# Kernel optimization log

Hardware: AMD Instinct MI355X
Metric: run time of the kernel (lower is better)

The kernel has to match this reference:

```python
import jax, jax.numpy as jnp
import numpy as np

B, V, E, L = 1024, 50000, 256, 17  # batch, nodeNum(vocab), embeddingSize, Huffman path length


def setup_inputs() -> dict:
    key = jax.random.key(0)
    k1, k2, k3, k4, k5 = jax.random.split(key, 5)
    x = jax.random.normal(k1, (B, V), dtype=jnp.float32)
    W = jax.random.normal(k2, (E, V), dtype=jnp.float32) * 0.02  # nn.Linear(nodeNum, embeddingSize).weight
    b = jax.random.normal(k3, (E,), dtype=jnp.float32) * 0.02    # nn.Linear bias
    path_vectors = jax.random.normal(k4, (B, L, E), dtype=jnp.float32)  # gathered treeNode.vector along each target's path
    path_signs = jax.random.randint(k5, (B, L), 0, 2, dtype=jnp.int32)  # 1 == 'left' (+v), 0 == 'right' (-v)
    return {"x": x, "W": W, "b": b, "path_vectors": path_vectors, "path_signs": path_signs}


def reference(x, W, b, path_vectors, path_signs):
    # x = self.embeddingSpace(x)
    emb = x @ W.T + b  # [B, E]
    # direct == 'left' -> +node.vector, 'right' -> -node.vector
    signs = (2 * path_signs - 1).astype(emb.dtype)  # [B, L] in {-1, +1}
    logits = jnp.einsum('ble,be->bl', path_vectors, emb) * signs  # per-node dot
    # output = prod_over_path sigmoid(dot)
    return jnp.prod(jax.nn.sigmoid(logits), axis=-1)  # [B]
```

## Files before the change

### kernel.cpp

```cpp
#include <hip/hip_runtime.h>
#include <hip/hip_bf16.h>
#include <math.h>

#define VDIM 50000
#define BDIM 1024
#define EDIM 256
#define LDIM 17

constexpr int BM = 128, BN = 128, BK = 32;
constexpr int KT_FULL = VDIM / BK;
constexpr int SPLITS  = 32;
constexpr int TAILZ   = KT_FULL % SPLITS;
constexpr int NBLK    = (EDIM / BN) * (BDIM / BM) * SPLITS;

typedef short bf16x8 __attribute__((ext_vector_type(8)));
typedef float f32x4  __attribute__((ext_vector_type(4)));

__device__ __forceinline__ void async_f4(const float* g, float* l) {
    __builtin_amdgcn_global_load_lds(
        (const __attribute__((address_space(1))) void*)g,
        (__attribute__((address_space(3))) void*)l, 16, 0, 0);
}

__device__ __forceinline__ void split8(const float4 f0, const float4 f1, bf16x8& h, bf16x8& l) {
    const float f[8] = {f0.x, f0.y, f0.z, f0.w, f1.x, f1.y, f1.z, f1.w};
#pragma unroll
    for (int i = 0; i < 8; ++i) {
        const uint32_t u  = __float_as_uint(f[i]);
        h[i] = (short)(u >> 16);
        const float lo = f[i] - __uint_as_float(u & 0xFFFF0000u);
        l[i] = (short)(__float_as_uint(lo) >> 16);
    }
}

__global__ __launch_bounds__(256) void gemm_split3(
    const float* __restrict__ X, const float* __restrict__ Wm,
    float* __restrict__ wsout, const int part) {
    __shared__ __align__(16) float sA[2][BM * BK];
    __shared__ __align__(16) float sB[2][BN * BK];

    const int tid = threadIdx.x;

    const int n   = blockIdx.x;
    const int r   = n & 7;
    const int q   = n >> 3;
    const int z   = (r << 2) + (q >> 4);
    const int t16 = q & 15;
    const int bn0 = (t16 & 1) * BN;
    const int bm0 = (t16 >> 1) * BM;

    const int lane = tid & 63;
    const int wv   = tid >> 6;
    const int wm0  = (wv >> 1) * 64;
    const int wn0  = (wv & 1) * 64;
    const int lm   = lane & 15;
    const int gk0  = (lane >> 4) * 2;

    const int rsub   = lane >> 3;
    const int grp    = lane & 7;
    const int coloff = ((grp ^ rsub) << 2);
    const int rowS   = wv * 32 + rsub;

    f32x4 acc[4][4] = {};

    auto issue = [&](int kt, int pb) {
        const int k0 = kt * BK;
#pragma unroll
        for (int j = 0; j < 4; ++j) {
            const int row = rowS + j * 8;
            async_f4(X  + (size_t)(bm0 + row) * VDIM + k0 + coloff, &sA[pb][(wv * 32 + j * 8) * BK]);
            async_f4(Wm + (size_t)(bn0 + row) * VDIM + k0 + coloff, &sB[pb][(wv * 32 + j * 8) * BK]);
        }
    };

    auto compute = [&](int pb) {
        const float* A = sA[pb];
        const float* Bs = sB[pb];
        bf16x8 ah[4], al[4];
#pragma unroll
        for (int mi = 0; mi < 4; ++mi) {
            const int row = wm0 + mi * 16 + lm;
            const int s = row & 7;
            const float4 f0 = *reinterpret_cast<const float4*>(&A[row * BK + ((gk0 ^ s) << 2)]);
            const float4 f1 = *reinterpret_cast<const float4*>(&A[row * BK + (((gk0 + 1) ^ s) << 2)]);
            split8(f0, f1, ah[mi], al[mi]);
        }
#pragma unroll
        for (int ni = 0; ni < 4; ++ni) {
            const int row = wn0 + ni * 16 + lm;
            const int s = row & 7;
            const float4 f0 = *reinterpret_cast<const float4*>(&Bs[row * BK + ((gk0 ^ s) << 2)]);
            const float4 f1 = *reinterpret_cast<const float4*>(&Bs[row * BK + (((gk0 + 1) ^ s) << 2)]);
            bf16x8 bh, bl;
            split8(f0, f1, bh, bl);
            __builtin_amdgcn_s_setprio(1);
#pragma unroll
            for (int mi = 0; mi < 4; ++mi) {
                acc[mi][ni] = __builtin_amdgcn_mfma_f32_16x16x32_bf16(ah[mi], bh, acc[mi][ni], 0, 0, 0);
                acc[mi][ni] = __builtin_amdgcn_mfma_f32_16x16x32_bf16(ah[mi], bl, acc[mi][ni], 0, 0, 0);
                acc[mi][ni] = __builtin_amdgcn_mfma_f32_16x16x32_bf16(al[mi], bh, acc[mi][ni], 0, 0, 0);
            }
            __builtin_amdgcn_s_setprio(0);
        }
    };

    int pb = 0;
    issue(z, 0);
    for (int kt = z + SPLITS; kt < KT_FULL; kt += SPLITS) {
        __syncthreads();
        issue(kt, pb ^ 1);
        compute(pb);
        pb ^= 1;
    }
    __syncthreads();
    compute(pb);

    if (z == TAILZ) {
        const int k0 = KT_FULL * BK;
#pragma unroll
        for (int j = 0; j < 4; ++j) {
            const int row = rowS + j * 8;
            float4 va = make_float4(0.f, 0.f, 0.f, 0.f), vb = va;
            if (coloff < 16) {
                va = *reinterpret_cast<const float4*>(X  + (size_t)(bm0 + row) * VDIM + k0 + coloff);
                vb = *reinterpret_cast<const float4*>(Wm + (size_t)(bn0 + row) * VDIM + k0 + coloff);
            }
            *reinterpret_cast<float4*>(&sA[pb ^ 1][row * BK + (grp << 2)]) = va;
            *reinterpret_cast<float4*>(&sB[pb ^ 1][row * BK + (grp << 2)]) = vb;
        }
        __syncthreads();
        compute(pb ^ 1);
    }

    const int orow = (lane >> 4) * 4;
    if (part) {
        float* dst = wsout + (size_t)z * BDIM * EDIM;
#pragma unroll
        for (int mi = 0; mi < 4; ++mi)
#pragma unroll
            for (int ni = 0; ni < 4; ++ni)
#pragma unroll
                for (int r2 = 0; r2 < 4; ++r2) {
                    const int gm = bm0 + wm0 + mi * 16 + orow + r2;
                    const int gn = bn0 + wn0 + ni * 16 + lm;
                    dst[(size_t)gm * EDIM + gn] = acc[mi][ni][r2];
                }
    } else {
#pragma unroll
        for (int mi = 0; mi < 4; ++mi)
#pragma unroll
            for (int ni = 0; ni < 4; ++ni)
#pragma unroll
                for (int r2 = 0; r2 < 4; ++r2) {
                    const int gm = bm0 + wm0 + mi * 16 + orow + r2;
                    const int gn = bn0 + wn0 + ni * 16 + lm;
                    atomicAdd(&wsout[gm * EDIM + gn], acc[mi][ni][r2]);
                }
    }
}

__global__ __launch_bounds__(256) void stage2_kernel(
    const float* __restrict__ ws, const float* __restrict__ bias,
    const float* __restrict__ pv, const int* __restrict__ signs,
    float* __restrict__ out, const int part) {
    const int b = blockIdx.x;
    __shared__ float se[EDIM];
    __shared__ float wp[4];
    const int t = threadIdx.x;
    float s = bias[t];
    if (part) {
#pragma unroll
        for (int zz = 0; zz < SPLITS; ++zz)
            s += ws[((size_t)zz * BDIM + b) * EDIM + t];
    } else {
        s += ws[b * EDIM + t];
    }
    se[t] = s;
    __syncthreads();
    const int w = t >> 6, lane = t & 63;
    float p = 1.0f;
    for (int l = w; l < LDIM; l += 4) {
        const float4 a = *reinterpret_cast<const float4*>(&pv[((size_t)b * LDIM + l) * EDIM + lane * 4]);
        const float4 e = *reinterpret_cast<const float4*>(&se[lane * 4]);
        float d = a.x * e.x + a.y * e.y + a.z * e.z + a.w * e.w;
#pragma unroll
        for (int off = 32; off > 0; off >>= 1) d += __shfl_xor(d, off, 64);
        const float zz = signs[b * LDIM + l] ? d : -d;
        p *= 1.0f / (1.0f + expf(-zz));
    }
    if (lane == 0) wp[w] = p;
    __syncthreads();
    if (t == 0) out[b] = wp[0] * wp[1] * wp[2] * wp[3];
}

extern "C" void kernel_launch(void* const* d_in, const int* in_sizes, int n_in,
                              void* d_out, int out_size, void* d_ws, size_t ws_size,
                              hipStream_t stream) {
    const float* X    = (const float*)d_in[0];
    const float* Wm   = (const float*)d_in[1];
    const float* bias = (const float*)d_in[2];
    const float* pv   = (const float*)d_in[3];
    const int*   sg   = (const int*)d_in[4];
    float* out = (float*)d_out;
    float* ws  = (float*)d_ws;

    const size_t need = (size_t)SPLITS * BDIM * EDIM * sizeof(float);
    const int part = (ws_size >= need) ? 1 : 0;

    if (!part)
        hipMemsetAsync(ws, 0, (size_t)BDIM * EDIM * sizeof(float), stream);

    gemm_split3<<<dim3(NBLK), 256, 0, stream>>>(X, Wm, ws, part);

    stage2_kernel<<<BDIM, 256, 0, stream>>>(ws, bias, pv, sg, out, part);
}
```

Baseline: 380.3 us.

## Drop LDS double buffering and double the split-K count

Replaces the double-buffered LDS pipeline with a single buffer, using a barrier before and after each async tile load. This halves shared memory per block so more blocks can be resident per CU. The split-K factor also goes from 32 to 64, giving 1024 blocks and a new z mapping. The trade-off is that loads no longer overlap compute inside a block, there is an extra barrier per tile, and the partial-sum workspace doubles, so the reduction in stage2 reads twice as much data. If the workspace is too small, the code falls back to atomics.

```diff
diff --git a/kernel.cpp b/kernel.cpp
--- a/kernel.cpp
+++ b/kernel.cpp
@@ -9,7 +9,7 @@
 
 constexpr int BM = 128, BN = 128, BK = 32;
 constexpr int KT_FULL = VDIM / BK;
-constexpr int SPLITS  = 32;
+constexpr int SPLITS  = 64;
 constexpr int TAILZ   = KT_FULL % SPLITS;
 constexpr int NBLK    = (EDIM / BN) * (BDIM / BM) * SPLITS;
 
@@ -36,15 +36,15 @@
 __global__ __launch_bounds__(256) void gemm_split3(
     const float* __restrict__ X, const float* __restrict__ Wm,
     float* __restrict__ wsout, const int part) {
-    __shared__ __align__(16) float sA[2][BM * BK];
-    __shared__ __align__(16) float sB[2][BN * BK];
+    __shared__ __align__(16) float sA[BM * BK];
+    __shared__ __align__(16) float sB[BN * BK];
 
     const int tid = threadIdx.x;
 
     const int n   = blockIdx.x;
     const int r   = n & 7;
     const int q   = n >> 3;
-    const int z   = (r << 2) + (q >> 4);
+    const int z   = (r << 3) + (q >> 4);
     const int t16 = q & 15;
     const int bn0 = (t16 & 1) * BN;
     const int bm0 = (t16 >> 1) * BM;
@@ -63,19 +63,19 @@
 
     f32x4 acc[4][4] = {};
 
-    auto issue = [&](int kt, int pb) {
+    auto issue = [&](int kt) {
         const int k0 = kt * BK;
 #pragma unroll
         for (int j = 0; j < 4; ++j) {
             const int row = rowS + j * 8;
-            async_f4(X  + (size_t)(bm0 + row) * VDIM + k0 + coloff, &sA[pb][(wv * 32 + j * 8) * BK]);
-            async_f4(Wm + (size_t)(bn0 + row) * VDIM + k0 + coloff, &sB[pb][(wv * 32 + j * 8) * BK]);
+            async_f4(X  + (size_t)(bm0 + row) * VDIM + k0 + coloff, &sA[(wv * 32 + j * 8) * BK]);
+            async_f4(Wm + (size_t)(bn0 + row) * VDIM + k0 + coloff, &sB[(wv * 32 + j * 8) * BK]);
         }
     };
 
-    auto compute = [&](int pb) {
-        const float* A = sA[pb];
-        const float* Bs = sB[pb];
+    auto compute = [&]() {
+        const float* A = sA;
+        const float* Bs = sB;
         bf16x8 ah[4], al[4];
 #pragma unroll
         for (int mi = 0; mi < 4; ++mi) {
@@ -104,19 +104,16 @@
         }
     };
 
-    int pb = 0;
-    issue(z, 0);
-    for (int kt = z + SPLITS; kt < KT_FULL; kt += SPLITS) {
-        __syncthreads();
-        issue(kt, pb ^ 1);
-        compute(pb);
-        pb ^= 1;
-    }
-    __syncthreads();
-    compute(pb);
+    for (int kt = z; kt < KT_FULL; kt += SPLITS) {
+        __syncthreads();
+        issue(kt);
+        __syncthreads();
+        compute();
+    }
 
     if (z == TAILZ) {
         const int k0 = KT_FULL * BK;
+        __syncthreads();
 #pragma unroll
         for (int j = 0; j < 4; ++j) {
             const int row = rowS + j * 8;
@@ -125,11 +122,11 @@
                 va = *reinterpret_cast<const float4*>(X  + (size_t)(bm0 + row) * VDIM + k0 + coloff);
                 vb = *reinterpret_cast<const float4*>(Wm + (size_t)(bn0 + row) * VDIM + k0 + coloff);
             }
-            *reinterpret_cast<float4*>(&sA[pb ^ 1][row * BK + (grp << 2)]) = va;
-            *reinterpret_cast<float4*>(&sB[pb ^ 1][row * BK + (grp << 2)]) = vb;
-        }
-        __syncthreads();
-        compute(pb ^ 1);
+            *reinterpret_cast<float4*>(&sA[row * BK + (grp << 2)]) = va;
+            *reinterpret_cast<float4*>(&sB[row * BK + (grp << 2)]) = vb;
+        }
+        __syncthreads();
+        compute();
     }
 
     const int orow = (lane >> 4) * 4;
```

Measured after the change: 416.3 us. 1.09x slower.
